# Kernel optimization log

Hardware: AMD Instinct MI355X
Metric: run time of the kernel (lower is better)

## Reference

```python
import jax, jax.numpy as jnp
import numpy as np

DIM = 512
QK_DIM = 128
HIDDEN = 2 * DIM  # expansion_factor * dim
EPS = 1e-5


def layernorm(x, scale, bias):
    mu = jnp.mean(x, axis=-1, keepdims=True)
    var = jnp.mean((x - mu) ** 2, axis=-1, keepdims=True)
    return (x - mu) * jax.lax.rsqrt(var + EPS) * scale + bias


def setup_inputs() -> dict:
    key = jax.random.key(0)
    ks = jax.random.split(key, 8)
    b, s = 4, 4096
    x = jax.random.normal(ks[0], (b, s, DIM), dtype=jnp.float32)
    inv = lambda fan_in: 1.0 / np.sqrt(fan_in)
    W_hidden = jax.random.normal(ks[1], (DIM, 2 * HIDDEN), dtype=jnp.float32) * inv(DIM)
    b_hidden = jnp.zeros((2 * HIDDEN,), dtype=jnp.float32)
    W_qk = jax.random.normal(ks[2], (DIM, QK_DIM), dtype=jnp.float32) * inv(DIM)
    b_qk = jnp.zeros((QK_DIM,), dtype=jnp.float32)
    gamma = jax.random.normal(ks[3], (2, QK_DIM), dtype=jnp.float32) * 0.02
    beta = jnp.zeros((2, QK_DIM), dtype=jnp.float32)
    W_out = jax.random.normal(ks[4], (HIDDEN, DIM), dtype=jnp.float32) * inv(HIDDEN)
    b_out = jnp.zeros((DIM,), dtype=jnp.float32)
    norm_scale = jnp.ones((DIM,), dtype=jnp.float32)
    norm_bias = jnp.zeros((DIM,), dtype=jnp.float32)
    return {
        "x": x,
        "norm_scale": norm_scale,
        "norm_bias": norm_bias,
        "W_hidden": W_hidden,
        "b_hidden": b_hidden,
        "W_qk": W_qk,
        "b_qk": b_qk,
        "gamma": gamma,
        "beta": beta,
        "W_out": W_out,
        "b_out": b_out,
    }


def reference(x, norm_scale, norm_bias, W_hidden, b_hidden, W_qk, b_qk, gamma, beta, W_out, b_out):
    seq_len = x.shape[-2]
    normed = layernorm(x, norm_scale, norm_bias)
    hidden = jax.nn.silu(normed @ W_hidden + b_hidden)          # [b, s, 2*hidden]
    v, gate = jnp.split(hidden, 2, axis=-1)                      # each [b, s, hidden]
    Z = jax.nn.silu(normed @ W_qk + b_qk)                        # [b, s, qk]
    QK = Z[..., None, :] * gamma + beta                          # [b, s, 2, qk]
    q = QK[..., 0, :]
    k = QK[..., 1, :]
    sim = jnp.einsum('bid,bjd->bij', q, k) / seq_len             # [b, s, s]
    A = jnp.square(jax.nn.relu(sim))
    V = jnp.einsum('bij,bjd->bid', A, v) * gate                  # [b, s, hidden]
    out = V @ W_out + b_out
    return out + x
```

## Files before the change

kernel.cpp:

```cpp
#include <hip/hip_runtime.h>
#include <cstdint>
#include <cstddef>

#define DIM   512
#define QKD   128
#define HID   1024
#define SEQ   4096
#define BAT   4
#define TOK   (BAT*SEQ)

typedef float f32x4 __attribute__((ext_vector_type(4)));
typedef int   i32x4 __attribute__((ext_vector_type(4)));
typedef int   i32x8 __attribute__((ext_vector_type(8)));

__device__ __forceinline__ float silu_f(float x) { return x / (1.f + __expf(-x)); }

__device__ __forceinline__ unsigned char f2e4(float f) {
    int v = __builtin_amdgcn_cvt_pk_fp8_f32(f, 0.f, 0, false);
    return (unsigned char)(v & 0xff);
}
__device__ __forceinline__ unsigned f2e4x4(float a, float b, float c, float d) {
    int w = __builtin_amdgcn_cvt_pk_fp8_f32(a, b, 0, false);
    w = __builtin_amdgcn_cvt_pk_fp8_f32(c, d, w, true);
    return (unsigned)w;
}
__device__ __forceinline__ float e42f(unsigned char b) {
    return __builtin_amdgcn_cvt_f32_fp8((int)b, 0);
}

__device__ __forceinline__ void load16_lds(const void* gp, void* lp) {
    __builtin_amdgcn_global_load_lds(
        (const __attribute__((address_space(1))) unsigned int*)gp,
        (__attribute__((address_space(3))) unsigned int*)lp,
        16, 0, 0);
}

#define WAITV6() asm volatile("s_waitcnt vmcnt(6)" ::: "memory")
#define WAITV0() asm volatile("s_waitcnt vmcnt(0)" ::: "memory")
#define FENCE()  do { asm volatile("" ::: "memory"); __builtin_amdgcn_sched_barrier(0); } while (0)

__global__ __launch_bounds__(256) void ln_kernel(
    const float* __restrict__ x, const float* __restrict__ sc,
    const float* __restrict__ bi, unsigned char* __restrict__ out)
{
    const int lane = threadIdx.x & 63, wid = threadIdx.x >> 6;
    const int row  = blockIdx.x * 4 + wid;
    const float4* xr = (const float4*)(x + (size_t)row * DIM);
    float4 a = xr[lane], b = xr[64 + lane];
    float s = a.x + a.y + a.z + a.w + b.x + b.y + b.z + b.w;
    float q = a.x*a.x + a.y*a.y + a.z*a.z + a.w*a.w
            + b.x*b.x + b.y*b.y + b.z*b.z + b.w*b.w;
#pragma unroll
    for (int m = 1; m < 64; m <<= 1) { s += __shfl_xor(s, m); q += __shfl_xor(q, m); }
    const float mean = s * (1.f / DIM);
    const float var  = q * (1.f / DIM) - mean * mean;
    const float rs   = rsqrtf(var + 1e-5f);
    float4 s0 = ((const float4*)sc)[lane], s1 = ((const float4*)sc)[64 + lane];
    float4 b0 = ((const float4*)bi)[lane], b1 = ((const float4*)bi)[64 + lane];
    unsigned wlo = f2e4x4((a.x - mean) * rs * s0.x + b0.x,
                          (a.y - mean) * rs * s0.y + b0.y,
                          (a.z - mean) * rs * s0.z + b0.z,
                          (a.w - mean) * rs * s0.w + b0.w);
    unsigned whi = f2e4x4((b.x - mean) * rs * s1.x + b1.x,
                          (b.y - mean) * rs * s1.y + b1.y,
                          (b.z - mean) * rs * s1.z + b1.z,
                          (b.w - mean) * rs * s1.w + b1.w);
    unsigned char* orow = out + (size_t)row * DIM;
    *(unsigned*)(orow + 4 * lane)       = wlo;
    *(unsigned*)(orow + 256 + 4 * lane) = whi;
}

__global__ __launch_bounds__(256) void tcast_f2e4_kernel(
    const float* __restrict__ in, unsigned char* __restrict__ out, int R, int C)
{
    __shared__ float t[32][33];
    const int tx = threadIdx.x & 31, ty = threadIdx.x >> 5;
    const int c0 = blockIdx.x * 32, r0 = blockIdx.y * 32;
#pragma unroll
    for (int i = 0; i < 4; ++i)
        t[ty + i * 8][tx] = in[(size_t)(r0 + ty + i * 8) * C + c0 + tx];
    __syncthreads();
#pragma unroll
    for (int i = 0; i < 4; ++i)
        out[(size_t)(c0 + ty + i * 8) * R + r0 + tx] = f2e4(t[tx][ty + i * 8] * 16.f);
}

__global__ __launch_bounds__(256) void copy_kernel(
    const float* __restrict__ in, float* __restrict__ out, int n4)
{
    int i = blockIdx.x * 256 + threadIdx.x;
    int stride = gridDim.x * 256;
    for (; i < n4; i += stride)
        ((float4*)out)[i] = ((const float4*)in)[i];
}

template<int EPI, int NX>
__global__ __launch_bounds__(256) void gemm8(
    const unsigned char* __restrict__ A, const unsigned char* __restrict__ B,
    int K, long strAz, long strBz, long strOz,
    const float* __restrict__ f0, const float* __restrict__ f1,
    const float* __restrict__ f2, const float* __restrict__ f3,
    const float* __restrict__ f4, const float* __restrict__ f5,
    unsigned char* __restrict__ gate,
    unsigned char* __restrict__ o0, unsigned char* __restrict__ o1,
    unsigned char* __restrict__ o2,
    float* __restrict__ fo, float scale)
{
    __shared__ unsigned char lds[32768];
    const int tid = threadIdx.x;
    const int d  = blockIdx.x + NX * blockIdx.y;
    const int qd = d >> 3;
    const int m0 = ((d & 7) + 8 * (qd / NX)) * 128;
    const int n0 = (qd % NX) * 128;
    const int z  = blockIdx.z;
    A += (size_t)z * strAz;  B += (size_t)z * strBz;
    const int lane = tid & 63, wid = tid >> 6;
    const int wm   = (wid & 1) * 64, wn = (wid >> 1) * 64;
    const int l15  = lane & 15, quad = lane >> 4;

    f32x4 acc[4][4] = {};

    const int srow = tid >> 3, sseg = tid & 7;
    const int gseg = sseg ^ (srow & 7);
    const unsigned char* gA = A + (size_t)(m0 + srow) * K + gseg * 16;
    const unsigned char* gB = B + (size_t)(n0 + srow) * K + gseg * 16;
    unsigned char* lA = lds + (size_t)tid * 16;
    unsigned char* lB = lds + 16384 + (size_t)tid * 16;

    const int olo = (((quad << 1) ^ (l15 & 7)) << 4);
    const int ohi = olo ^ 16;

    for (int kt = 0; kt < K; kt += 128) {
#pragma unroll
        for (int i = 0; i < 4; ++i)
            load16_lds(gA + (size_t)i * 32 * K + kt, lA + i * 4096);
#pragma unroll
        for (int i = 0; i < 4; ++i)
            load16_lds(gB + (size_t)i * 32 * K + kt, lB + i * 4096);
        __syncthreads();
        i32x4 alo[4], ahi[4], blo[4], bhi[4];
#pragma unroll
        for (int mi = 0; mi < 4; ++mi) {
            const unsigned char* p = lds + (wm + mi * 16 + l15) * 128;
            alo[mi] = *(const i32x4*)(p + olo); ahi[mi] = *(const i32x4*)(p + ohi);
        }
#pragma unroll
        for (int ni = 0; ni < 4; ++ni) {
            const unsigned char* p = lds + 16384 + (wn + ni * 16 + l15) * 128;
            blo[ni] = *(const i32x4*)(p + olo); bhi[ni] = *(const i32x4*)(p + ohi);
        }
#pragma unroll
        for (int mi = 0; mi < 4; ++mi) {
            i32x8 af = __builtin_shufflevector(alo[mi], ahi[mi], 0,1,2,3,4,5,6,7);
#pragma unroll
            for (int ni = 0; ni < 4; ++ni) {
                i32x8 bf = __builtin_shufflevector(blo[ni], bhi[ni], 0,1,2,3,4,5,6,7);
                acc[mi][ni] = __builtin_amdgcn_mfma_scale_f32_16x16x128_f8f6f4(
                    af, bf, acc[mi][ni], 0, 0,
                    0, 0x7F7F7F7F, 0, 0x7F7F7F7F);
            }
        }
        __syncthreads();
    }

#pragma unroll
    for (int mi = 0; mi < 4; ++mi)
#pragma unroll
    for (int ni = 0; ni < 4; ++ni) {
        const int grow0 = m0 + wm + mi * 16 + quad * 4;
        const int gcol  = n0 + wn + ni * 16 + l15;
        if constexpr (EPI == 1) {
            unsigned char* Ao = o0 + (size_t)z * strOz;
#pragma unroll
            for (int r = 0; r < 4; ++r) {
                float t = fmaxf(acc[mi][ni][r], 0.f) * 0.0625f;
                Ao[(size_t)(grow0 + r) * SEQ + gcol] = f2e4(t * t);
            }
        }
    }
}

template<int EPI, int NX>
__global__ __launch_bounds__(512, 2) void gemm8p(
    const unsigned char* __restrict__ A, const unsigned char* __restrict__ B,
    int K, long strAz, long strBz, long strOz,
    const float* __restrict__ f0, const float* __restrict__ f1,
    const float* __restrict__ f2, const float* __restrict__ f3,
    const float* __restrict__ f4, const float* __restrict__ f5,
    unsigned char* __restrict__ gate,
    unsigned char* __restrict__ o0, unsigned char* __restrict__ o1,
    unsigned char* __restrict__ o2,
    float* __restrict__ fo, float scale)
{
    __shared__ unsigned char lds[3 * 49152];
    const int tid = threadIdx.x;
    const int d  = blockIdx.x + NX * blockIdx.y;
    const int qd = d >> 3;
    const int m0 = ((d & 7) + 8 * (qd / NX)) * 256;
    const int n0 = (qd % NX) * 128;
    const int z  = blockIdx.z;
    A += (size_t)z * strAz;  B += (size_t)z * strBz;
    const int lane = tid & 63, wid = tid >> 6;
    const int wm   = (wid & 3) * 64, wn = (wid >> 2) * 64;
    const int l15  = lane & 15, quad = lane >> 4;

    f32x4 acc[4][4] = {};

    const int srow = tid >> 3, sseg = tid & 7;
    const int gseg = sseg ^ (srow & 7);
    const unsigned char* gAs = A + (size_t)(m0 + srow) * K + gseg * 16;
    const unsigned char* gBs = B + (size_t)(n0 + srow) * K + gseg * 16;

    const int olo = (((quad << 1) ^ (l15 & 7)) << 4);
    const int ohi = olo ^ 16;

    const int NT = K >> 7;

    auto STAGE = [&](int t, int buf) {
        const size_t ko = (size_t)t << 7;
        unsigned char* lb = lds + buf * 49152 + tid * 16;
#pragma unroll
        for (int i = 0; i < 4; ++i)
            load16_lds(gAs + (size_t)(i * 64) * K + ko, lb + i * 8192);
#pragma unroll
        for (int i = 0; i < 2; ++i)
            load16_lds(gBs + (size_t)(i * 64) * K + ko, lb + 32768 + i * 8192);
    };

    auto COMPUTE = [&](int buf) {
        const unsigned char* la = lds + buf * 49152;
        const unsigned char* lb = la + 32768;
        i32x4 alo[4], ahi[4], blo[4], bhi[4];
#pragma unroll
        for (int mi = 0; mi < 4; ++mi) {
            const unsigned char* p = la + (size_t)(wm + mi * 16 + l15) * 128;
            alo[mi] = *(const i32x4*)(p + olo); ahi[mi] = *(const i32x4*)(p + ohi);
        }
#pragma unroll
        for (int ni = 0; ni < 4; ++ni) {
            const unsigned char* p = lb + (size_t)(wn + ni * 16 + l15) * 128;
            blo[ni] = *(const i32x4*)(p + olo); bhi[ni] = *(const i32x4*)(p + ohi);
        }
#pragma unroll
        for (int mi = 0; mi < 4; ++mi) {
            i32x8 af = __builtin_shufflevector(alo[mi], ahi[mi], 0,1,2,3,4,5,6,7);
#pragma unroll
            for (int ni = 0; ni < 4; ++ni) {
                i32x8 bf = __builtin_shufflevector(blo[ni], bhi[ni], 0,1,2,3,4,5,6,7);
                acc[mi][ni] = __builtin_amdgcn_mfma_scale_f32_16x16x128_f8f6f4(
                    af, bf, acc[mi][ni], 0, 0,
                    0, 0x7F7F7F7F, 0, 0x7F7F7F7F);
            }
        }
    };

    STAGE(0, 0);
    if (NT > 1) { STAGE(1, 1); WAITV6(); }
    else        {              WAITV0(); }
    __builtin_amdgcn_s_barrier();
    FENCE();

    int cbuf = 0, sbuf = 2;
    for (int t = 0; t < NT; ++t) {
        if (t + 2 < NT) STAGE(t + 2, sbuf);
        COMPUTE(cbuf);
        if (t + 1 < NT) {
            if (t + 2 < NT) WAITV6(); else WAITV0();
            __builtin_amdgcn_s_barrier();
            FENCE();
        }
        cbuf = (cbuf == 2) ? 0 : cbuf + 1;
        sbuf = (sbuf == 2) ? 0 : sbuf + 1;
    }

#pragma unroll
    for (int mi = 0; mi < 4; ++mi)
#pragma unroll
    for (int ni = 0; ni < 4; ++ni) {
        const int grow0 = m0 + wm + mi * 16 + quad * 4;
        const int gcol  = n0 + wn + ni * 16 + l15;
        if constexpr (EPI == 0) {
            if (gcol < HID) {
                const int b = grow0 >> 12, rloc = grow0 & (SEQ - 1);
                unsigned w = f2e4x4(silu_f(acc[mi][ni][0] * 0.0625f + f0[gcol]),
                                    silu_f(acc[mi][ni][1] * 0.0625f + f0[gcol]),
                                    silu_f(acc[mi][ni][2] * 0.0625f + f0[gcol]),
                                    silu_f(acc[mi][ni][3] * 0.0625f + f0[gcol]));
                *(unsigned*)(o0 + (size_t)b * HID * SEQ + (size_t)gcol * SEQ + rloc) = w;
            } else if (gcol < 2048) {
#pragma unroll
                for (int r = 0; r < 4; ++r)
                    gate[(size_t)(grow0 + r) * HID + (gcol - HID)] =
                        f2e4(silu_f(acc[mi][ni][r] * 0.0625f + f0[gcol]));
            } else {
                const int c = gcol - 2048;
#pragma unroll
                for (int r = 0; r < 4; ++r) {
                    float zf = silu_f(acc[mi][ni][r] * 0.0625f + f1[c]);
                    o1[(size_t)(grow0 + r) * QKD + c] = f2e4((zf * f2[c] + f4[c]) * 64.f);
                    o2[(size_t)(grow0 + r) * QKD + c] = f2e4((zf * f3[c] + f5[c]) * 64.f);
                }
            }
        } else if constexpr (EPI == 1) {
            unsigned char* Ao = o0 + (size_t)z * strOz;
#pragma unroll
            for (int r = 0; r < 4; ++r) {
                float t = fmaxf(acc[mi][ni][r], 0.f) * 0.0625f;
                Ao[(size_t)(grow0 + r) * SEQ + gcol] = f2e4(t * t);
            }
        } else if constexpr (EPI == 2) {
            unsigned char* gz = gate + (size_t)z * strOz;
            unsigned char* vo = o0 + (size_t)z * strOz;
#pragma unroll
            for (int r = 0; r < 4; ++r) {
                float g = e42f(gz[(size_t)(grow0 + r) * HID + gcol]);
                vo[(size_t)(grow0 + r) * HID + gcol] = f2e4(acc[mi][ni][r] * scale * g);
            }
        } else {
#pragma unroll
            for (int r = 0; r < 4; ++r)
                fo[(size_t)(grow0 + r) * DIM + gcol] =
                    acc[mi][ni][r] * scale + f0[gcol] + f1[(size_t)(grow0 + r) * DIM + gcol];
        }
    }
}

extern "C" void kernel_launch(void* const* d_in, const int* in_sizes, int n_in,
                              void* d_out, int out_size, void* d_ws, size_t ws_size,
                              hipStream_t stream) {
    const float* x     = (const float*)d_in[0];
    const float* nsc   = (const float*)d_in[1];
    const float* nbi   = (const float*)d_in[2];
    const float* Wh    = (const float*)d_in[3];
    const float* bh    = (const float*)d_in[4];
    const float* Wqk   = (const float*)d_in[5];
    const float* bqk   = (const float*)d_in[6];
    const float* gamma = (const float*)d_in[7];
    const float* beta  = (const float*)d_in[8];
    const float* Wout  = (const float*)d_in[9];
    const float* bout  = (const float*)d_in[10];
    float* out = (float*)d_out;

    uint8_t* ws = (uint8_t*)d_ws;
    size_t off = 0;
    auto alloc = [&](size_t n) { uint8_t* p = ws + off; off += (n + 255) & ~(size_t)255; return p; };
    unsigned char* normed8 = (unsigned char*)alloc((size_t)TOK * DIM);
    unsigned char* Wc8     = (unsigned char*)alloc((size_t)2176 * DIM);
    unsigned char* Wout8   = (unsigned char*)alloc((size_t)DIM * HID);
    unsigned char* vT8     = (unsigned char*)alloc((size_t)BAT * HID * SEQ);
    unsigned char* gbuf    = (unsigned char*)alloc((size_t)TOK * HID);
    unsigned char* q8      = (unsigned char*)alloc((size_t)TOK * QKD);
    unsigned char* k8      = (unsigned char*)alloc((size_t)TOK * QKD);
    unsigned char* Ab8     = (unsigned char*)alloc((size_t)BAT * SEQ * SEQ);
    unsigned char* vg8     = (unsigned char*)alloc((size_t)TOK * HID);

    if (ws_size < off) {
        copy_kernel<<<4096, 256, 0, stream>>>(x, out, TOK * DIM / 4);
        return;
    }

    ln_kernel<<<TOK / 4, 256, 0, stream>>>(x, nsc, nbi, normed8);
    tcast_f2e4_kernel<<<dim3(2048 / 32, DIM / 32), 256, 0, stream>>>(Wh, Wc8, DIM, 2048);
    tcast_f2e4_kernel<<<dim3(QKD / 32, DIM / 32), 256, 0, stream>>>(
        Wqk, Wc8 + (size_t)2048 * DIM, DIM, QKD);
    tcast_f2e4_kernel<<<dim3(DIM / 32, HID / 32), 256, 0, stream>>>(Wout, Wout8, HID, DIM);

    gemm8p<0, 17><<<dim3(17, TOK / 256), 512, 0, stream>>>(
        normed8, Wc8, DIM, 0, 0, 0,
        bh, bqk, gamma, gamma + QKD, beta, beta + QKD,
        gbuf, vT8, q8, k8, nullptr, 0.f);

    gemm8<1, 32><<<dim3(SEQ / 128, SEQ / 128, BAT), 256, 0, stream>>>(
        q8, k8, QKD, (long)SEQ * QKD, (long)SEQ * QKD, (long)SEQ * SEQ,
        nullptr, nullptr, nullptr, nullptr, nullptr, nullptr,
        nullptr, Ab8, nullptr, nullptr, nullptr, 0.f);

    gemm8p<2, 8><<<dim3(HID / 128, SEQ / 256, BAT), 512, 0, stream>>>(
        Ab8, vT8, SEQ, (long)SEQ * SEQ, (long)HID * SEQ, (long)SEQ * HID,
        nullptr, nullptr, nullptr, nullptr, nullptr, nullptr,
        gbuf, vg8, nullptr, nullptr, nullptr, 0x1p-12f);

    gemm8p<3, 4><<<dim3(DIM / 128, TOK / 256), 512, 0, stream>>>(
        vg8, Wout8, HID, 0, 0, 0,
        bout, x, nullptr, nullptr, nullptr, nullptr,
        nullptr, nullptr, nullptr, nullptr, out, 0x1p-32f);
}
```

Measured before the change: 280.9 us.

## Use a 256x256 FP8 MFMA tile kernel for the attention-times-V GEMM

Adds a dedicated gemm9p kernel that computes 256x256 output tiles, with 8x4 MFMA accumulators per wave and a double-buffered 128-wide K stage in 128KB of LDS. It replaces the 256x128-tile launch for the A·V GEMM, which halves the number of blocks and raises operand reuse per byte loaded. It also deletes the now-unused EPI==1 branch from gemm8p. The trade-offs are that the large LDS footprint allows only one block per CU, and the grid becomes a single wave of 256 blocks, which limits latency hiding.

```diff
diff --git a/kernel.cpp b/kernel.cpp
--- a/kernel.cpp
+++ b/kernel.cpp
@@ -35,6 +35,7 @@
         16, 0, 0);
 }
 
+#define WAITV8() asm volatile("s_waitcnt vmcnt(8)" ::: "memory")
 #define WAITV6() asm volatile("s_waitcnt vmcnt(6)" ::: "memory")
 #define WAITV0() asm volatile("s_waitcnt vmcnt(0)" ::: "memory")
 #define FENCE()  do { asm volatile("" ::: "memory"); __builtin_amdgcn_sched_barrier(0); } while (0)
@@ -301,13 +302,6 @@
                     o2[(size_t)(grow0 + r) * QKD + c] = f2e4((zf * f3[c] + f5[c]) * 64.f);
                 }
             }
-        } else if constexpr (EPI == 1) {
-            unsigned char* Ao = o0 + (size_t)z * strOz;
-#pragma unroll
-            for (int r = 0; r < 4; ++r) {
-                float t = fmaxf(acc[mi][ni][r], 0.f) * 0.0625f;
-                Ao[(size_t)(grow0 + r) * SEQ + gcol] = f2e4(t * t);
-            }
         } else if constexpr (EPI == 2) {
             unsigned char* gz = gate + (size_t)z * strOz;
             unsigned char* vo = o0 + (size_t)z * strOz;
@@ -316,11 +310,108 @@
                 float g = e42f(gz[(size_t)(grow0 + r) * HID + gcol]);
                 vo[(size_t)(grow0 + r) * HID + gcol] = f2e4(acc[mi][ni][r] * scale * g);
             }
-        } else {
+        } else if constexpr (EPI == 3) {
 #pragma unroll
             for (int r = 0; r < 4; ++r)
                 fo[(size_t)(grow0 + r) * DIM + gcol] =
                     acc[mi][ni][r] * scale + f0[gcol] + f1[(size_t)(grow0 + r) * DIM + gcol];
+        }
+    }
+}
+
+template<int EPI, int NX>
+__global__ __launch_bounds__(512, 2) void gemm9p(
+    const unsigned char* __restrict__ A, const unsigned char* __restrict__ B,
+    int K, long strAz, long strBz, long strOz,
+    unsigned char* __restrict__ gate,
+    unsigned char* __restrict__ o0, float scale)
+{
+    __shared__ unsigned char lds[2 * 65536];
+    const int tid = threadIdx.x;
+    const int d  = blockIdx.x + NX * blockIdx.y;
+    const int qd = d >> 3;
+    const int m0 = ((d & 7) + 8 * (qd / NX)) * 256;
+    const int n0 = (qd % NX) * 256;
+    const int z  = blockIdx.z;
+    A += (size_t)z * strAz;  B += (size_t)z * strBz;
+    const int lane = tid & 63, wid = tid >> 6;
+    const int wm   = (wid & 1) * 128, wn = (wid >> 1) * 64;
+    const int l15  = lane & 15, quad = lane >> 4;
+
+    f32x4 acc[8][4] = {};
+
+    const int srow = tid >> 3, sseg = tid & 7;
+    const int gseg = sseg ^ (srow & 7);
+    const unsigned char* gAs = A + (size_t)(m0 + srow) * K + gseg * 16;
+    const unsigned char* gBs = B + (size_t)(n0 + srow) * K + gseg * 16;
+
+    const int olo = (((quad << 1) ^ (l15 & 7)) << 4);
+    const int ohi = olo ^ 16;
+
+    const int NT = K >> 7;
+
+    auto STAGE = [&](int t, int buf) {
+        const size_t ko = (size_t)t << 7;
+        unsigned char* lb = lds + buf * 65536 + tid * 16;
+#pragma unroll
+        for (int i = 0; i < 4; ++i)
+            load16_lds(gAs + (size_t)(i * 64) * K + ko, lb + i * 8192);
+#pragma unroll
+        for (int i = 0; i < 4; ++i)
+            load16_lds(gBs + (size_t)(i * 64) * K + ko, lb + 32768 + i * 8192);
+    };
+
+    auto COMPUTE = [&](int buf) {
+        const unsigned char* la = lds + buf * 65536;
+        const unsigned char* lb = la + 32768;
+        i32x8 bf[4];
+#pragma unroll
+        for (int ni = 0; ni < 4; ++ni) {
+            const unsigned char* p = lb + (size_t)(wn + ni * 16 + l15) * 128;
+            i32x4 lo = *(const i32x4*)(p + olo), hi = *(const i32x4*)(p + ohi);
+            bf[ni] = __builtin_shufflevector(lo, hi, 0,1,2,3,4,5,6,7);
+        }
+#pragma unroll
+        for (int mi = 0; mi < 8; ++mi) {
+            const unsigned char* p = la + (size_t)(wm + mi * 16 + l15) * 128;
+            i32x4 lo = *(const i32x4*)(p + olo), hi = *(const i32x4*)(p + ohi);
+            i32x8 af = __builtin_shufflevector(lo, hi, 0,1,2,3,4,5,6,7);
+#pragma unroll
+            for (int ni = 0; ni < 4; ++ni)
+                acc[mi][ni] = __builtin_amdgcn_mfma_scale_f32_16x16x128_f8f6f4(
+                    af, bf[ni], acc[mi][ni], 0, 0,
+                    0, 0x7F7F7F7F, 0, 0x7F7F7F7F);
+        }
+    };
+
+    STAGE(0, 0);
+    for (int t = 0; t < NT; ++t) {
+        const int cb = t & 1;
+        if (t + 1 < NT) { STAGE(t + 1, cb ^ 1); WAITV8(); }
+        else            {                       WAITV0(); }
+        __builtin_amdgcn_s_barrier();
+        FENCE();
+        COMPUTE(cb);
+        if (t + 1 < NT) {
+            __builtin_amdgcn_s_barrier();
+            FENCE();
+        }
+    }
+
+#pragma unroll
+    for (int mi = 0; mi < 8; ++mi)
+#pragma unroll
+    for (int ni = 0; ni < 4; ++ni) {
+        const int grow0 = m0 + wm + mi * 16 + quad * 4;
+        const int gcol  = n0 + wn + ni * 16 + l15;
+        if constexpr (EPI == 2) {
+            unsigned char* gz = gate + (size_t)z * strOz;
+            unsigned char* vo = o0 + (size_t)z * strOz;
+#pragma unroll
+            for (int r = 0; r < 4; ++r) {
+                float g = e42f(gz[(size_t)(grow0 + r) * HID + gcol]);
+                vo[(size_t)(grow0 + r) * HID + gcol] = f2e4(acc[mi][ni][r] * scale * g);
+            }
         }
     }
 }
@@ -375,10 +466,9 @@
         nullptr, nullptr, nullptr, nullptr, nullptr, nullptr,
         nullptr, Ab8, nullptr, nullptr, nullptr, 0.f);
 
-    gemm8p<2, 8><<<dim3(HID / 128, SEQ / 256, BAT), 512, 0, stream>>>(
+    gemm9p<2, 4><<<dim3(HID / 256, SEQ / 256, BAT), 512, 0, stream>>>(
         Ab8, vT8, SEQ, (long)SEQ * SEQ, (long)HID * SEQ, (long)SEQ * HID,
-        nullptr, nullptr, nullptr, nullptr, nullptr, nullptr,
-        gbuf, vg8, nullptr, nullptr, nullptr, 0x1p-12f);
+        gbuf, vg8, 0x1p-12f);
 
     gemm8p<3, 4><<<dim3(DIM / 128, TOK / 256), 512, 0, stream>>>(
         vg8, Wout8, HID, 0, 0, 0,
```

Result: no change. 282.6 us (+0.6%).
